# Kernel optimization log

Hardware: AMD Instinct MI355X
Metric: run time of the kernel (lower is better)

## Reference

```python
import jax, jax.numpy as jnp
import numpy as np

N = 1_000_000   # total atoms in batched graph
G = 50_000      # number of molecules (graphs)
F = 128         # gnn_out_feats (node feature dim)
H = 128         # classifier_hidden_feats
T = 12          # n_tasks
EPS = 1e-5      # BatchNorm1d eps


def setup_inputs() -> dict:
    key = jax.random.key(0)
    ks = jax.random.split(key, 20)
    s = 0.05
    inp = {}
    inp["node_feats"] = jax.random.normal(ks[0], (N, F), jnp.float32)
    inp["segment_ids"] = jnp.sort(jax.random.randint(ks[1], (N,), 0, G))
    inp["num_graphs"] = G
    # per-task atom weighting: Linear(F,1) per task, stacked -> [T,F]
    inp["atom_w"] = jax.random.normal(ks[2], (T, F), jnp.float32) * s
    inp["atom_b"] = jnp.zeros((T,), jnp.float32)
    # fc_layer 1: Linear(F,H) -> ReLU -> BatchNorm1d(H) (eval mode)
    inp["W1"] = jax.random.normal(ks[3], (T, F, H), jnp.float32) * s
    inp["b1"] = jnp.zeros((T, H), jnp.float32)
    inp["g1"] = jnp.ones((T, H), jnp.float32)
    inp["be1"] = jnp.zeros((T, H), jnp.float32)
    inp["rm1"] = jnp.zeros((T, H), jnp.float32)
    inp["rv1"] = jnp.ones((T, H), jnp.float32)
    # fc_layer 2 and 3: Linear(H,H) -> ReLU -> BatchNorm1d(H)
    inp["W2"] = jax.random.normal(ks[4], (T, H, H), jnp.float32) * s
    inp["b2"] = jnp.zeros((T, H), jnp.float32)
    inp["g2"] = jnp.ones((T, H), jnp.float32)
    inp["be2"] = jnp.zeros((T, H), jnp.float32)
    inp["rm2"] = jnp.zeros((T, H), jnp.float32)
    inp["rv2"] = jnp.ones((T, H), jnp.float32)
    inp["W3"] = jax.random.normal(ks[5], (T, H, H), jnp.float32) * s
    inp["b3"] = jnp.zeros((T, H), jnp.float32)
    inp["g3"] = jnp.ones((T, H), jnp.float32)
    inp["be3"] = jnp.zeros((T, H), jnp.float32)
    inp["rm3"] = jnp.zeros((T, H), jnp.float32)
    inp["rv3"] = jnp.ones((T, H), jnp.float32)
    # output_layer: Linear(H,H) -> ReLU -> Linear(H,1)
    inp["oW1"] = jax.random.normal(ks[6], (T, H, H), jnp.float32) * s
    inp["ob1"] = jnp.zeros((T, H), jnp.float32)
    inp["oW2"] = jax.random.normal(ks[7], (T, H), jnp.float32) * s
    inp["ob2"] = jnp.zeros((T,), jnp.float32)
    return inp


def _fc(x, W, b, g, be, rm, rv):
    # Linear -> ReLU -> BatchNorm1d (eval, running stats), batched over tasks t
    y = jax.nn.relu(jnp.einsum('gti,tio->gto', x, W) + b)
    return (y - rm) * (g * jax.lax.rsqrt(rv + EPS)) + be


def reference(node_feats, segment_ids, num_graphs, atom_w, atom_b,
              W1, b1, g1, be1, rm1, rv1,
              W2, b2, g2, be2, rm2, rv2,
              W3, b3, g3, be3, rm3, rv3,
              oW1, ob1, oW2, ob2):
    n_tasks = atom_w.shape[0]
    # WeightAndSum: per-task sigmoid node weights [N,T]
    w = jax.nn.sigmoid(node_feats @ atom_w.T + atom_b)
    # per-task weighted segment-sum pooling: loop over small fixed task count
    sums = [jax.ops.segment_sum(node_feats * w[:, t:t + 1], segment_ids,
                                num_segments=num_graphs)
            for t in range(n_tasks)]
    mol = jnp.stack(sums, axis=1)  # [G, T, F]
    h = _fc(mol, W1, b1, g1, be1, rm1, rv1)
    h = _fc(h, W2, b2, g2, be2, rm2, rv2)
    h = _fc(h, W3, b3, g3, be3, rm3, rv3)
    z = jax.nn.relu(jnp.einsum('gth,tho->gto', h, oW1) + ob1)
    pred = jnp.einsum('gth,th->gt', z, oW2) + ob2  # [G, T]
    return pred
```

## Files before the change

### kernel.cpp

```cpp
#include <hip/hip_runtime.h>
#include <hip/hip_bf16.h>
#include <hip/hip_fp16.h>

typedef _Float16 f16;
typedef _Float16 f16x2 __attribute__((ext_vector_type(2)));
typedef _Float16 f16x4 __attribute__((ext_vector_type(4)));
typedef _Float16 f16x8 __attribute__((ext_vector_type(8)));
typedef float f32x4 __attribute__((ext_vector_type(4)));

#define BN_EPS 1e-5f

__global__ void seg_starts_k(const int* __restrict__ seg, int N, int G, int* __restrict__ start) {
    int n = blockIdx.x * blockDim.x + threadIdx.x;
    if (n >= N) return;
    int s = seg[n];
    int p = (n == 0) ? -1 : seg[n - 1];
    for (int g = p + 1; g <= s; ++g) start[g] = n;
    if (n == N - 1) {
        for (int g = s + 1; g <= G; ++g) start[g] = N;
    }
}

__global__ void prep_k(const float* __restrict__ W1, const float* __restrict__ b1,
                       const float* __restrict__ W2, const float* __restrict__ b2,
                       const float* __restrict__ W3, const float* __restrict__ b3,
                       const float* __restrict__ oW1, const float* __restrict__ ob1,
                       const float* __restrict__ g1, const float* __restrict__ be1,
                       const float* __restrict__ rm1, const float* __restrict__ rv1,
                       const float* __restrict__ g2, const float* __restrict__ be2,
                       const float* __restrict__ rm2, const float* __restrict__ rv2,
                       const float* __restrict__ g3, const float* __restrict__ be3,
                       const float* __restrict__ rm3, const float* __restrict__ rv3,
                       f16* __restrict__ Wt, float* __restrict__ bp) {
    int T = gridDim.x;
    int t = blockIdx.x, l = blockIdx.y;
    int o = threadIdx.x;
    __shared__ float s_sh[128], c_sh[128];

    const float *W, *b, *gg = nullptr, *be = nullptr, *rm = nullptr, *rv = nullptr;
    if (l == 0)      { W = W1;  b = b1; }
    else if (l == 1) { W = W2;  b = b2;  gg = g1; be = be1; rm = rm1; rv = rv1; }
    else if (l == 2) { W = W3;  b = b3;  gg = g2; be = be2; rm = rm2; rv = rv2; }
    else             { W = oW1; b = ob1; gg = g3; be = be3; rm = rm3; rv = rv3; }

    float s = 1.f, c = 0.f;
    if (gg) {
        float sv = gg[t * 128 + o] * rsqrtf(rv[t * 128 + o] + BN_EPS);
        s = sv;
        c = be[t * 128 + o] - rm[t * 128 + o] * sv;
    }
    s_sh[o] = s;
    c_sh[o] = c;
    __syncthreads();

    const float* Wsrc = W + (size_t)t * 128 * 128;
    f16* Wdst = Wt + (((size_t)l * T + t) * 128 + o) * 128;
    float acc = b[t * 128 + o];
    for (int i = 0; i < 128; ++i) {
        float wv = Wsrc[i * 128 + o];
        Wdst[i] = (f16)(s_sh[i] * wv);
        acc += c_sh[i] * wv;
    }
    bp[((size_t)l * T + t) * 128 + o] = acc;
}

__global__ __launch_bounds__(256) void pool5_k(const float* __restrict__ feats,
                                               const float* __restrict__ atom_w,
                                               const float* __restrict__ atom_b,
                                               const int* __restrict__ start,
                                               f16* __restrict__ mol, int G) {
    int wave = threadIdx.x >> 6, lane = threadIdx.x & 63;
    int g = blockIdx.x * 4 + wave;
    if (g >= G) return;
    int lr = lane & 15, kg = lane >> 4;

    f16x8 bfr[4];
    float ab = 0.f;
#pragma unroll
    for (int ks = 0; ks < 4; ++ks) {
        f16x8 v = {};
        if (lr < 12) {
            const float* s = atom_w + lr * 128 + ks * 32 + kg * 8;
#pragma unroll
            for (int j = 0; j < 8; ++j) v[j] = (f16)s[j];
        }
        bfr[ks] = v;
    }
    if (lr < 12) ab = atom_b[lr];

    f32x4 acc[8];
#pragma unroll
    for (int nf = 0; nf < 8; ++nf) acc[nf] = (f32x4){0.f, 0.f, 0.f, 0.f};

    int s = start[g], e = start[g + 1];

    for (int c0 = s; c0 < e; c0 += 16) {
        int rB[4];
#pragma unroll
        for (int j = 0; j < 4; ++j) {
            int a = c0 + (kg << 2) + j;
            rB[j] = (a < e) ? a : (e - 1);
        }
        float bx[8][4];
#pragma unroll
        for (int j = 0; j < 4; ++j) {
            const float* pB = feats + (size_t)rB[j] * 128 + lr;
#pragma unroll
            for (int fb = 0; fb < 8; ++fb) bx[fb][j] = pB[fb << 4];
        }

        int rA = c0 + lr; if (rA >= e) rA = e - 1;
        const float* pA = feats + (size_t)rA * 128 + (kg << 3);
        f32x4 pa = {0.f, 0.f, 0.f, 0.f};
#pragma unroll
        for (int ks = 0; ks < 4; ++ks) {
            float4 u0 = *(const float4*)(pA + (ks << 5));
            float4 u1 = *(const float4*)(pA + (ks << 5) + 4);
            f16x8 afr;
            afr[0] = (f16)u0.x; afr[1] = (f16)u0.y; afr[2] = (f16)u0.z; afr[3] = (f16)u0.w;
            afr[4] = (f16)u1.x; afr[5] = (f16)u1.y; afr[6] = (f16)u1.z; afr[7] = (f16)u1.w;
            pa = __builtin_amdgcn_mfma_f32_16x16x32_f16(afr, bfr[ks], pa, 0, 0, 0);
        }

        f16x4 a2;
#pragma unroll
        for (int j = 0; j < 4; ++j) {
            float w = 1.f / (1.f + __expf(-(pa[j] + ab)));
            int a = c0 + (kg << 2) + j;
            a2[j] = (a < e) ? (f16)w : (f16)0.f;
        }

#pragma unroll
        for (int fb = 0; fb < 8; ++fb) {
            f16x4 b2;
#pragma unroll
            for (int j = 0; j < 4; ++j) b2[j] = (f16)bx[fb][j];
            acc[fb] = __builtin_amdgcn_mfma_f32_16x16x16f16(a2, b2, acc[fb], 0, 0, 0);
        }
    }

    if (kg < 3) {
#pragma unroll
        for (int fb = 0; fb < 8; ++fb)
#pragma unroll
            for (int j = 0; j < 4; ++j)
                mol[((size_t)((kg << 2) + j) * G + g) * 128 + (fb << 4) + lr] =
                    (f16)acc[fb][j];
    }
}

__global__ __launch_bounds__(256, 2) void fc_k(const f16* __restrict__ mol,
                                               const f16* __restrict__ Wt,
                                               const float* __restrict__ bp,
                                               const float* __restrict__ oW2,
                                               const float* __restrict__ ob2,
                                               float* __restrict__ out, int G, int T) {
    __shared__ f16 A[2][64][128];
    __shared__ f16 B[128][128];

    int t = blockIdx.y;
    int g0 = blockIdx.x * 64;
    int tid = threadIdx.x;

    {
        const f16* src = mol + (size_t)t * G * 128;
#pragma unroll
        for (int k = 0; k < 4; ++k) {
            int c = tid + k * 256;
            int r = c >> 4, sl = c & 15;
            uint4 v = make_uint4(0u, 0u, 0u, 0u);
            if (g0 + r < G) v = *(const uint4*)(src + (size_t)(g0 + r) * 128 + sl * 8);
            *(uint4*)(&A[0][r][(sl ^ (r & 7)) * 8]) = v;
        }
    }
    {
        const f16* src = Wt + ((size_t)0 * T + t) * 128 * 128;
#pragma unroll
        for (int k = 0; k < 8; ++k) {
            int c = tid + k * 256;
            int r = c >> 4, sl = c & 15;
            uint4 v = *(const uint4*)(src + (size_t)r * 128 + sl * 8);
            *(uint4*)(&B[r][(sl ^ (r & 7)) * 8]) = v;
        }
    }
    __syncthreads();

    int wid = tid >> 6, lane = tid & 63;
    int lg = lane >> 4, lr = lane & 15;
    int m0 = wid * 16;
    int arow = m0 + lr;
    float pred[4] = {0.f, 0.f, 0.f, 0.f};
    int cur = 0;

    for (int l = 0; l < 4; ++l) {
        f16x8 afr[4];
#pragma unroll
        for (int ks = 0; ks < 4; ++ks) {
            int sl = (4 * ks + lg) ^ (arow & 7);
            afr[ks] = *(const f16x8*)(&A[cur][arow][sl * 8]);
        }
        const float* bias = bp + ((size_t)l * T + t) * 128;
#pragma unroll
        for (int nf = 0; nf < 8; ++nf) {
            int n = nf * 16 + lr;
            f32x4 acc = {0.f, 0.f, 0.f, 0.f};
#pragma unroll
            for (int ks = 0; ks < 4; ++ks) {
                int sl = (4 * ks + lg) ^ (n & 7);
                f16x8 bfr = *(const f16x8*)(&B[n][sl * 8]);
                acc = __builtin_amdgcn_mfma_f32_16x16x32_f16(afr[ks], bfr, acc, 0, 0, 0);
            }
            float bv = bias[n];
            if (l < 3) {
#pragma unroll
                for (int j = 0; j < 4; ++j) {
                    float y = acc[j] + bv;
                    y = y > 0.f ? y : 0.f;
                    int rr = m0 + 4 * lg + j;
                    A[cur ^ 1][rr][(((n >> 3) ^ (rr & 7)) << 3) + (n & 7)] = (f16)y;
                }
            } else {
                float w2 = oW2[t * 128 + n];
#pragma unroll
                for (int j = 0; j < 4; ++j) {
                    float z = acc[j] + bv;
                    z = z > 0.f ? z : 0.f;
                    pred[j] += z * w2;
                }
            }
        }
        __syncthreads();
        if (l < 3) {
            const f16* src = Wt + ((size_t)(l + 1) * T + t) * 128 * 128;
#pragma unroll
            for (int k = 0; k < 8; ++k) {
                int c = tid + k * 256;
                int r = c >> 4, sl = c & 15;
                uint4 v = *(const uint4*)(src + (size_t)r * 128 + sl * 8);
                *(uint4*)(&B[r][(sl ^ (r & 7)) * 8]) = v;
            }
            __syncthreads();
            cur ^= 1;
        }
    }

#pragma unroll
    for (int m = 1; m < 16; m <<= 1) {
#pragma unroll
        for (int j = 0; j < 4; ++j) pred[j] += __shfl_xor(pred[j], m, 64);
    }
    if (lr == 0) {
        float ob = ob2[t];
#pragma unroll
        for (int j = 0; j < 4; ++j) {
            int gg = g0 + m0 + 4 * lg + j;
            if (gg < G) out[(size_t)gg * T + t] = pred[j] + ob;
        }
    }
}

extern "C" void kernel_launch(void* const* d_in, const int* in_sizes, int n_in,
                              void* d_out, int out_size, void* d_ws, size_t ws_size,
                              hipStream_t stream) {
    const float* node_feats = (const float*)d_in[0];
    const int*   seg        = (const int*)d_in[1];
    const float* atom_w     = (const float*)d_in[3];
    const float* atom_b     = (const float*)d_in[4];
    const float* W1  = (const float*)d_in[5];
    const float* b1  = (const float*)d_in[6];
    const float* g1  = (const float*)d_in[7];
    const float* be1 = (const float*)d_in[8];
    const float* rm1 = (const float*)d_in[9];
    const float* rv1 = (const float*)d_in[10];
    const float* W2  = (const float*)d_in[11];
    const float* b2  = (const float*)d_in[12];
    const float* g2  = (const float*)d_in[13];
    const float* be2 = (const float*)d_in[14];
    const float* rm2 = (const float*)d_in[15];
    const float* rv2 = (const float*)d_in[16];
    const float* W3  = (const float*)d_in[17];
    const float* b3  = (const float*)d_in[18];
    const float* g3  = (const float*)d_in[19];
    const float* be3 = (const float*)d_in[20];
    const float* rm3 = (const float*)d_in[21];
    const float* rv3 = (const float*)d_in[22];
    const float* oW1 = (const float*)d_in[23];
    const float* ob1 = (const float*)d_in[24];
    const float* oW2 = (const float*)d_in[25];
    const float* ob2 = (const float*)d_in[26];

    int T = in_sizes[4];
    int F = in_sizes[3] / T;
    int N = in_sizes[0] / F;
    int G = out_size / T;

    char* ws = (char*)d_ws;
    size_t off = 0;
    int* start = (int*)ws;
    off += (((size_t)(G + 1) * 4) + 255) & ~(size_t)255;
    f16* Wt = (f16*)(ws + off);
    off += (((size_t)4 * T * 128 * 128 * 2) + 255) & ~(size_t)255;
    float* bp = (float*)(ws + off);
    off += (((size_t)4 * T * 128 * 4) + 255) & ~(size_t)255;
    f16* mol = (f16*)(ws + off);

    seg_starts_k<<<(N + 255) / 256, 256, 0, stream>>>(seg, N, G, start);
    prep_k<<<dim3(T, 4), 128, 0, stream>>>(W1, b1, W2, b2, W3, b3, oW1, ob1,
                                           g1, be1, rm1, rv1,
                                           g2, be2, rm2, rv2,
                                           g3, be3, rm3, rv3, Wt, bp);
    pool5_k<<<(G + 3) / 4, 256, 0, stream>>>(node_feats, atom_w, atom_b, start, mol, G);
    fc_k<<<dim3((G + 63) / 64, T), 256, 0, stream>>>(mol, Wt, bp, oW2, ob2,
                                                     (float*)d_out, G, T);
}
```

Baseline: 387.4 us.

## Use direct global-to-LDS loads with pre-swizzled layouts in fused MLP kernel

```diff
diff --git a/kernel.cpp b/kernel.cpp
--- a/kernel.cpp
+++ b/kernel.cpp
@@ -7,6 +7,9 @@
 typedef _Float16 f16x4 __attribute__((ext_vector_type(4)));
 typedef _Float16 f16x8 __attribute__((ext_vector_type(8)));
 typedef float f32x4 __attribute__((ext_vector_type(4)));
+
+typedef __attribute__((address_space(1))) const void gas_t;
+typedef __attribute__((address_space(3))) void las_t;
 
 #define BN_EPS 1e-5f
 
@@ -58,7 +61,7 @@
     float acc = b[t * 128 + o];
     for (int i = 0; i < 128; ++i) {
         float wv = Wsrc[i * 128 + o];
-        Wdst[i] = (f16)(s_sh[i] * wv);
+        Wdst[(((i >> 3) ^ (o & 7)) << 3) + (i & 7)] = (f16)(s_sh[i] * wv);
         acc += c_sh[i] * wv;
     }
     bp[((size_t)l * T + t) * 128 + o] = acc;
@@ -140,65 +143,70 @@
     }
 
     if (kg < 3) {
-#pragma unroll
-        for (int fb = 0; fb < 8; ++fb)
+        int gx = g & 7;
+#pragma unroll
+        for (int fb = 0; fb < 8; ++fb) {
+            int slot = (fb << 1) + (lr >> 3);
+            int fi = (((slot ^ gx)) << 3) + (lr & 7);
 #pragma unroll
             for (int j = 0; j < 4; ++j)
-                mol[((size_t)((kg << 2) + j) * G + g) * 128 + (fb << 4) + lr] =
-                    (f16)acc[fb][j];
-    }
-}
-
-__global__ __launch_bounds__(256, 2) void fc_k(const f16* __restrict__ mol,
+                mol[((size_t)((kg << 2) + j) * G + g) * 128 + fi] = (f16)acc[fb][j];
+        }
+    }
+}
+
+__global__ __launch_bounds__(256, 3) void fc_k(const f16* __restrict__ mol,
                                                const f16* __restrict__ Wt,
                                                const float* __restrict__ bp,
                                                const float* __restrict__ oW2,
                                                const float* __restrict__ ob2,
                                                float* __restrict__ out, int G, int T) {
-    __shared__ f16 A[2][64][128];
+    __shared__ f16 A[64][128];
     __shared__ f16 B[128][128];
 
     int t = blockIdx.y;
     int g0 = blockIdx.x * 64;
     int tid = threadIdx.x;
+    int wid = tid >> 6, lane = tid & 63;
 
     {
-        const f16* src = mol + (size_t)t * G * 128;
-#pragma unroll
-        for (int k = 0; k < 4; ++k) {
-            int c = tid + k * 256;
-            int r = c >> 4, sl = c & 15;
-            uint4 v = make_uint4(0u, 0u, 0u, 0u);
-            if (g0 + r < G) v = *(const uint4*)(src + (size_t)(g0 + r) * 128 + sl * 8);
-            *(uint4*)(&A[0][r][(sl ^ (r & 7)) * 8]) = v;
-        }
-    }
-    {
-        const f16* src = Wt + ((size_t)0 * T + t) * 128 * 128;
-#pragma unroll
-        for (int k = 0; k < 8; ++k) {
-            int c = tid + k * 256;
-            int r = c >> 4, sl = c & 15;
-            uint4 v = *(const uint4*)(src + (size_t)r * 128 + sl * 8);
-            *(uint4*)(&B[r][(sl ^ (r & 7)) * 8]) = v;
-        }
-    }
-    __syncthreads();
-
-    int wid = tid >> 6, lane = tid & 63;
+        const f16* aplane = mol + (size_t)t * G * 128;
+#pragma unroll
+        for (int i = 0; i < 4; ++i) {
+            int c = wid + (i << 2);
+            int r = (c << 2) + (lane >> 4);
+            int row = g0 + r; if (row >= G) row = G - 1;
+            const f16* src = aplane + (size_t)row * 128 + ((lane & 15) << 3);
+            __builtin_amdgcn_global_load_lds((gas_t*)src,
+                (las_t*)((char*)&A[0][0] + c * 1024), 16, 0, 0);
+        }
+        const f16* bsrc = Wt + ((size_t)0 * T + t) * 16384;
+#pragma unroll
+        for (int i = 0; i < 8; ++i) {
+            int c = wid + (i << 2);
+            int r = (c << 2) + (lane >> 4);
+            const f16* src = bsrc + (size_t)r * 128 + ((lane & 15) << 3);
+            __builtin_amdgcn_global_load_lds((gas_t*)src,
+                (las_t*)((char*)&B[0][0] + c * 1024), 16, 0, 0);
+        }
+    }
+
     int lg = lane >> 4, lr = lane & 15;
     int m0 = wid * 16;
     int arow = m0 + lr;
     float pred[4] = {0.f, 0.f, 0.f, 0.f};
-    int cur = 0;
 
     for (int l = 0; l < 4; ++l) {
+        asm volatile("s_waitcnt vmcnt(0)" ::: "memory");
+        __syncthreads();
+
         f16x8 afr[4];
 #pragma unroll
         for (int ks = 0; ks < 4; ++ks) {
             int sl = (4 * ks + lg) ^ (arow & 7);
-            afr[ks] = *(const f16x8*)(&A[cur][arow][sl * 8]);
-        }
+            afr[ks] = *(const f16x8*)(&A[arow][sl * 8]);
+        }
+
         const float* bias = bp + ((size_t)l * T + t) * 128;
 #pragma unroll
         for (int nf = 0; nf < 8; ++nf) {
@@ -217,7 +225,7 @@
                     float y = acc[j] + bv;
                     y = y > 0.f ? y : 0.f;
                     int rr = m0 + 4 * lg + j;
-                    A[cur ^ 1][rr][(((n >> 3) ^ (rr & 7)) << 3) + (n & 7)] = (f16)y;
+                    A[rr][(((n >> 3) ^ (rr & 7)) << 3) + (n & 7)] = (f16)y;
                 }
             } else {
                 float w2 = oW2[t * 128 + n];
@@ -231,16 +239,15 @@
         }
         __syncthreads();
         if (l < 3) {
-            const f16* src = Wt + ((size_t)(l + 1) * T + t) * 128 * 128;
-#pragma unroll
-            for (int k = 0; k < 8; ++k) {
-                int c = tid + k * 256;
-                int r = c >> 4, sl = c & 15;
-                uint4 v = *(const uint4*)(src + (size_t)r * 128 + sl * 8);
-                *(uint4*)(&B[r][(sl ^ (r & 7)) * 8]) = v;
+            const f16* bsrc = Wt + ((size_t)(l + 1) * T + t) * 16384;
+#pragma unroll
+            for (int i = 0; i < 8; ++i) {
+                int c = wid + (i << 2);
+                int r = (c << 2) + (lane >> 4);
+                const f16* src = bsrc + (size_t)r * 128 + ((lane & 15) << 3);
+                __builtin_amdgcn_global_load_lds((gas_t*)src,
+                    (las_t*)((char*)&B[0][0] + c * 1024), 16, 0, 0);
             }
-            __syncthreads();
-            cur ^= 1;
         }
     }
 
```

Measured after the change: 348.8 us. 10.0% less time.
